# Optimization experiments

Measured on AMD Instinct MI355X. Metric: run time of the kernel, lower is better.

## Reference

```python
import jax, jax.numpy as jnp
import numpy as np

T, HW, C = 64, 24, 1024
MID = 256
WIN = 2  # 'video' forward_type -> 2x2 windows


def setup_inputs() -> dict:
    key = jax.random.key(0)
    k1, k2, k3, k4, k5 = jax.random.split(key, 5)
    return {
        "image_features": jax.random.normal(k1, (T, HW * HW, C), dtype=jnp.float32),
        "Wq": jax.random.normal(k2, (C, MID), dtype=jnp.float32) * 0.02,
        "bq": jax.random.normal(k3, (MID,), dtype=jnp.float32) * 0.02,
        "Wk": jax.random.normal(k4, (C, MID), dtype=jnp.float32) * 0.02,
        "bk": jax.random.normal(k5, (MID,), dtype=jnp.float32) * 0.02,
    }


def reference(image_features, Wq, bq, Wk, bk):
    # forward_type == 'video': 2x2 windowed attention over pooled patches
    t, n, c = image_features.shape
    H = W = int(np.sqrt(n))
    h2, w2 = H // WIN, W // WIN
    # [T, H, W, C] -> [T, h2, 2, w2, 2, C] -> [T, h2, w2, 2, 2, C] -> [T, P, 4, C]
    x = image_features.reshape(t, h2, WIN, w2, WIN, c)
    windows = x.transpose(0, 1, 3, 2, 4, 5).reshape(t, h2 * w2, WIN * WIN, c)
    # avg_pool2d(2,2) == mean over each 2x2 window
    pooled = windows.mean(axis=2)  # [T, P, C]
    q = pooled @ Wq + bq           # [T, P, MID]
    k = windows @ Wk + bk          # [T, P, 4, MID]
    scale = 1.0 / jnp.sqrt(jnp.float32(MID))
    attn = jnp.einsum("tpd,tpwd->tpw", q, k) * scale  # [T, P, 4]
    attn = jnp.nan_to_num(attn)
    attn = jax.nn.softmax(attn, axis=-1)
    attn_feat = jnp.einsum("tpw,tpwc->tpc", attn, windows)  # softmax-weighted value avg
    # query dim has size 1, so .mean(1) in torch is identity here
    return pooled + attn_feat  # [T, P, C]; new_image_size = (h2, w2) is static
```

## Files before the change

kernel.cpp:

```cpp
#include <hip/hip_runtime.h>

#define T_ 64
#define P_ 144
#define NPAIR 9216
#define C_ 1024
#define MID_ 256
#define NKROW 36864

typedef __attribute__((ext_vector_type(4))) float f32x4;
typedef __attribute__((ext_vector_type(8))) __bf16 bf16x8;
typedef __attribute__((ext_vector_type(4))) __bf16 bf16x4;

__device__ __forceinline__ void async_copy16(const void* g, void* l) {
  __builtin_amdgcn_global_load_lds(
      (const __attribute__((address_space(1))) unsigned int*)g,
      (__attribute__((address_space(3))) unsigned int*)l, 16, 0, 0);
}

__global__ void pool_convert_kernel(const float* __restrict__ img,
                                    __bf16* __restrict__ winb,
                                    __bf16* __restrict__ poolb) {
  const int pair = blockIdx.x;
  const int t = pair / P_;
  const int p = pair - t * P_;
  const int wy = p / 12, wx = p - wy * 12;
  const int c = threadIdx.x * 4;
  const float* base = img + (size_t)t * 576 * C_;
  const int r0 = 48 * wy + 2 * wx;
  const int rows[4] = {r0, r0 + 1, r0 + 24, r0 + 25};
  f32x4 s = {0.f, 0.f, 0.f, 0.f};
#pragma unroll
  for (int w = 0; w < 4; ++w) {
    f32x4 v = *(const f32x4*)(base + (size_t)rows[w] * C_ + c);
    s += v;
    bf16x4 bv;
#pragma unroll
    for (int j = 0; j < 4; ++j) bv[j] = (__bf16)v[j];
    *(bf16x4*)(winb + ((size_t)pair * 4 + w) * C_ + c) = bv;
  }
  s *= 0.25f;
  bf16x4 pv;
#pragma unroll
  for (int j = 0; j < 4; ++j) pv[j] = (__bf16)s[j];
  *(bf16x4*)(poolb + (size_t)pair * C_ + c) = pv;
}

__global__ void wtrans_kernel(const float* __restrict__ Wq,
                              const float* __restrict__ Wk,
                              __bf16* __restrict__ Wqt,
                              __bf16* __restrict__ Wkt) {
  __shared__ float t[32][33];
  const float* src = blockIdx.z ? Wk : Wq;
  __bf16* dst = blockIdx.z ? Wkt : Wqt;
  const int k0 = blockIdx.x * 32, n0 = blockIdx.y * 32;
#pragma unroll
  for (int i = 0; i < 32; i += 8) {
    t[threadIdx.y + i][threadIdx.x] =
        src[(size_t)(k0 + threadIdx.y + i) * MID_ + n0 + threadIdx.x];
  }
  __syncthreads();
#pragma unroll
  for (int i = 0; i < 32; i += 8) {
    dst[(size_t)(n0 + threadIdx.y + i) * C_ + k0 + threadIdx.x] =
        (__bf16)t[threadIdx.x][threadIdx.y + i];
  }
}

__global__ __launch_bounds__(256) void gemm_qk_kernel(
    const __bf16* __restrict__ Apool, const __bf16* __restrict__ Awin,
    const __bf16* __restrict__ Bqt, const __bf16* __restrict__ Bkt,
    const float* __restrict__ bq, const float* __restrict__ bk,
    float* __restrict__ Qo, float* __restrict__ Ko) {
  __shared__ __align__(16) __bf16 As[128 * 32];
  __shared__ __align__(16) __bf16 Bs[128 * 32];
  const int bid = blockIdx.x;
  const __bf16* A;
  const __bf16* Bt;
  const float* bias;
  float* Cout;
  int mt, nt;
  if (bid < 144) {
    A = Apool; Bt = Bqt; bias = bq; Cout = Qo;
    mt = bid >> 1; nt = bid & 1;
  } else {
    const int b = bid - 144;
    A = Awin; Bt = Bkt; bias = bk; Cout = Ko;
    mt = b >> 1; nt = b & 1;
  }
  const int tid = threadIdx.x;
  const int lane = tid & 63;
  const int wv = tid >> 6;
  const int quad = lane >> 4, lr = lane & 15;
  const int wm = wv >> 1, wn = wv & 1;

  const int r0 = tid >> 2, p0 = tid & 3;
  const __bf16* ga0 = A + ((size_t)mt * 128 + r0) * (size_t)C_ + p0 * 8;
  const __bf16* ga1 = ga0 + (size_t)64 * C_;
  const __bf16* gb0 = Bt + ((size_t)nt * 128 + r0) * (size_t)C_ + p0 * 8;
  const __bf16* gb1 = gb0 + (size_t)64 * C_;
  const int wvb = (tid & ~63) * 16;
  char* AsB0 = (char*)As + wvb;
  char* AsB1 = (char*)As + 4096 + wvb;
  char* BsB0 = (char*)Bs + wvb;
  char* BsB1 = (char*)Bs + 4096 + wvb;

  f32x4 acc[4][4] = {};

  for (int it = 0; it < 32; ++it) {
    async_copy16(ga0, AsB0);
    async_copy16(ga1, AsB1);
    async_copy16(gb0, BsB0);
    async_copy16(gb1, BsB1);
    ga0 += 32; ga1 += 32; gb0 += 32; gb1 += 32;
    __syncthreads();

    bf16x8 a[4], b[4];
    const bf16x8* Ap = (const bf16x8*)As;
    const bf16x8* Bp = (const bf16x8*)Bs;
#pragma unroll
    for (int i = 0; i < 4; ++i) {
      a[i] = Ap[(wm * 64 + i * 16 + lr) * 4 + quad];
      b[i] = Bp[(wn * 64 + i * 16 + lr) * 4 + quad];
    }
#pragma unroll
    for (int mi = 0; mi < 4; ++mi)
#pragma unroll
      for (int ni = 0; ni < 4; ++ni)
        acc[mi][ni] = __builtin_amdgcn_mfma_f32_16x16x32_bf16(
            a[mi], b[ni], acc[mi][ni], 0, 0, 0);
    __syncthreads();
  }

  const int colb = nt * 128 + wn * 64;
  const int rowb = mt * 128 + wm * 64 + quad * 4;
#pragma unroll
  for (int ni = 0; ni < 4; ++ni) {
    const int col = colb + ni * 16 + lr;
    const float bv = bias[col];
#pragma unroll
    for (int mi = 0; mi < 4; ++mi) {
      const int row = rowb + mi * 16;
#pragma unroll
      for (int r = 0; r < 4; ++r)
        Cout[(size_t)(row + r) * MID_ + col] = acc[mi][ni][r] + bv;
    }
  }
}

__global__ void attn_epilogue_kernel(const float* __restrict__ Qm,
                                     const float* __restrict__ Km,
                                     const __bf16* __restrict__ winb,
                                     const __bf16* __restrict__ poolb,
                                     float* __restrict__ out) {
  const int pair = blockIdx.x;
  const int tid = threadIdx.x;
  const int wv = tid >> 6, lane = tid & 63;
  __shared__ float red[4][4];
  const float qv = Qm[(size_t)pair * MID_ + tid];
#pragma unroll
  for (int w = 0; w < 4; ++w) {
    float p = qv * Km[((size_t)pair * 4 + w) * MID_ + tid];
    p += __shfl_down(p, 32);
    p += __shfl_down(p, 16);
    p += __shfl_down(p, 8);
    p += __shfl_down(p, 4);
    p += __shfl_down(p, 2);
    p += __shfl_down(p, 1);
    if (lane == 0) red[w][wv] = p;
  }
  __syncthreads();
  float lg[4];
  float mx = -1e30f;
#pragma unroll
  for (int w = 0; w < 4; ++w) {
    lg[w] = (red[w][0] + red[w][1] + red[w][2] + red[w][3]) * 0.0625f;
    mx = fmaxf(mx, lg[w]);
  }
  float att[4];
  float ssum = 0.f;
#pragma unroll
  for (int w = 0; w < 4; ++w) {
    att[w] = __expf(lg[w] - mx);
    ssum += att[w];
  }
  const float inv = 1.f / ssum;

  const int c = tid * 4;
  const bf16x4 pv = *(const bf16x4*)(poolb + (size_t)pair * C_ + c);
  f32x4 o;
#pragma unroll
  for (int j = 0; j < 4; ++j) o[j] = (float)pv[j];
#pragma unroll
  for (int w = 0; w < 4; ++w) {
    const float aw = att[w] * inv;
    const bf16x4 wvv = *(const bf16x4*)(winb + ((size_t)pair * 4 + w) * C_ + c);
#pragma unroll
    for (int j = 0; j < 4; ++j) o[j] += aw * (float)wvv[j];
  }
  *(f32x4*)(out + (size_t)pair * C_ + c) = o;
}

extern "C" void kernel_launch(void* const* d_in, const int* in_sizes, int n_in,
                              void* d_out, int out_size, void* d_ws,
                              size_t ws_size, hipStream_t stream) {
  const float* img = (const float*)d_in[0];
  const float* Wq = (const float*)d_in[1];
  const float* bq = (const float*)d_in[2];
  const float* Wk = (const float*)d_in[3];
  const float* bk = (const float*)d_in[4];
  float* out = (float*)d_out;

  char* ws = (char*)d_ws;
  __bf16* winb = (__bf16*)ws;
  __bf16* poolb = (__bf16*)(ws + 75497472);
  __bf16* Wqt = (__bf16*)(ws + 94371840);
  __bf16* Wkt = (__bf16*)(ws + 94896128);
  float* Qo = (float*)(ws + 95420416);
  float* Ko = (float*)(ws + 104857600);

  pool_convert_kernel<<<NPAIR, 256, 0, stream>>>(img, winb, poolb);
  wtrans_kernel<<<dim3(32, 8, 2), dim3(32, 8, 1), 0, stream>>>(Wq, Wk, Wqt, Wkt);
  gemm_qk_kernel<<<720, 256, 0, stream>>>(poolb, winb, Wqt, Wkt, bq, bk, Qo, Ko);
  attn_epilogue_kernel<<<NPAIR, 256, 0, stream>>>(Qo, Ko, winb, poolb, out);
}
```

Before: 299.2 us.

## Drop bf16 window copy; convert fp32 image inside K GEMM and epilogue

Removes the materialized bf16 windows buffer. The K-projection GEMM now loads fp32 image rows directly and converts them to bf16 in registers before writing LDS. The output kernel reads the fp32 image to compute both the pooled mean and the weighted sum. Pooling and weight transposition are merged into one launch, and Q/K are stored as bf16 to halve that traffic. The K GEMM A-path switches from async LDS copies to synchronous register loads, which may expose more latency, and Q/K precision drops.

```diff
diff --git a/kernel.cpp b/kernel.cpp
--- a/kernel.cpp
+++ b/kernel.cpp
@@ -5,7 +5,6 @@
 #define NPAIR 9216
 #define C_ 1024
 #define MID_ 256
-#define NKROW 36864
 
 typedef __attribute__((ext_vector_type(4))) float f32x4;
 typedef __attribute__((ext_vector_type(8))) __bf16 bf16x8;
@@ -17,74 +16,96 @@
       (__attribute__((address_space(3))) unsigned int*)l, 16, 0, 0);
 }
 
-__global__ void pool_convert_kernel(const float* __restrict__ img,
-                                    __bf16* __restrict__ winb,
-                                    __bf16* __restrict__ poolb) {
-  const int pair = blockIdx.x;
+__device__ __forceinline__ int img_row_of(int g) {
+  const int pair = g >> 2;
+  const int w = g & 3;
   const int t = pair / P_;
-  const int p = pair - t * P_;
-  const int wy = p / 12, wx = p - wy * 12;
-  const int c = threadIdx.x * 4;
-  const float* base = img + (size_t)t * 576 * C_;
-  const int r0 = 48 * wy + 2 * wx;
-  const int rows[4] = {r0, r0 + 1, r0 + 24, r0 + 25};
-  f32x4 s = {0.f, 0.f, 0.f, 0.f};
-#pragma unroll
-  for (int w = 0; w < 4; ++w) {
-    f32x4 v = *(const f32x4*)(base + (size_t)rows[w] * C_ + c);
-    s += v;
-    bf16x4 bv;
-#pragma unroll
-    for (int j = 0; j < 4; ++j) bv[j] = (__bf16)v[j];
-    *(bf16x4*)(winb + ((size_t)pair * 4 + w) * C_ + c) = bv;
-  }
-  s *= 0.25f;
-  bf16x4 pv;
-#pragma unroll
-  for (int j = 0; j < 4; ++j) pv[j] = (__bf16)s[j];
-  *(bf16x4*)(poolb + (size_t)pair * C_ + c) = pv;
-}
-
-__global__ void wtrans_kernel(const float* __restrict__ Wq,
-                              const float* __restrict__ Wk,
-                              __bf16* __restrict__ Wqt,
-                              __bf16* __restrict__ Wkt) {
-  __shared__ float t[32][33];
-  const float* src = blockIdx.z ? Wk : Wq;
-  __bf16* dst = blockIdx.z ? Wkt : Wqt;
-  const int k0 = blockIdx.x * 32, n0 = blockIdx.y * 32;
-#pragma unroll
-  for (int i = 0; i < 32; i += 8) {
-    t[threadIdx.y + i][threadIdx.x] =
-        src[(size_t)(k0 + threadIdx.y + i) * MID_ + n0 + threadIdx.x];
-  }
-  __syncthreads();
-#pragma unroll
-  for (int i = 0; i < 32; i += 8) {
-    dst[(size_t)(n0 + threadIdx.y + i) * C_ + k0 + threadIdx.x] =
-        (__bf16)t[threadIdx.x][threadIdx.y + i];
-  }
+  const int pp = pair - t * P_;
+  const int wy = pp / 12, wx = pp - wy * 12;
+  return t * 576 + 48 * wy + 2 * wx + (w >> 1) * 24 + (w & 1);
+}
+
+__global__ void prep_kernel(const float* __restrict__ img,
+                            const float* __restrict__ Wq,
+                            const float* __restrict__ Wk,
+                            __bf16* __restrict__ poolb,
+                            __bf16* __restrict__ Wqt,
+                            __bf16* __restrict__ Wkt) {
+  const int bid = blockIdx.x;
+  const int tid = threadIdx.x;
+  if (bid < NPAIR) {
+    const int t = bid / P_;
+    const int p = bid - t * P_;
+    const int wy = p / 12, wx = p - wy * 12;
+    const int c = tid * 4;
+    const float* base = img + ((size_t)t * 576 + 48 * wy + 2 * wx) * C_;
+    f32x4 s = *(const f32x4*)(base + c);
+    s += *(const f32x4*)(base + (size_t)1 * C_ + c);
+    s += *(const f32x4*)(base + (size_t)24 * C_ + c);
+    s += *(const f32x4*)(base + (size_t)25 * C_ + c);
+    s *= 0.25f;
+    bf16x4 pv;
+#pragma unroll
+    for (int j = 0; j < 4; ++j) pv[j] = (__bf16)s[j];
+    *(bf16x4*)(poolb + (size_t)bid * C_ + c) = pv;
+  } else {
+    __shared__ float tl[32][33];
+    const int b = bid - NPAIR;
+    const int bx = b & 31;
+    const int by = (b >> 5) & 7;
+    const int bz = b >> 8;
+    const float* src = bz ? Wk : Wq;
+    __bf16* dst = bz ? Wkt : Wqt;
+    const int tx = tid & 31, ty = tid >> 5;
+    const int k0 = bx * 32, n0 = by * 32;
+#pragma unroll
+    for (int i = 0; i < 32; i += 8)
+      tl[ty + i][tx] = src[(size_t)(k0 + ty + i) * MID_ + n0 + tx];
+    __syncthreads();
+#pragma unroll
+    for (int i = 0; i < 32; i += 8)
+      dst[(size_t)(n0 + ty + i) * C_ + k0 + tx] = (__bf16)tl[tx][ty + i];
+  }
+}
+
+__device__ __forceinline__ void mfma_tile(const __bf16* As, const __bf16* Bs,
+                                          int wm, int wn, int quad, int lr,
+                                          f32x4 acc[4][4]) {
+  bf16x8 a[4], b[4];
+  const bf16x8* Ap = (const bf16x8*)As;
+  const bf16x8* Bp = (const bf16x8*)Bs;
+#pragma unroll
+  for (int i = 0; i < 4; ++i) {
+    a[i] = Ap[(wm * 64 + i * 16 + lr) * 4 + quad];
+    b[i] = Bp[(wn * 64 + i * 16 + lr) * 4 + quad];
+  }
+#pragma unroll
+  for (int mi = 0; mi < 4; ++mi)
+#pragma unroll
+    for (int ni = 0; ni < 4; ++ni)
+      acc[mi][ni] = __builtin_amdgcn_mfma_f32_16x16x32_bf16(
+          a[mi], b[ni], acc[mi][ni], 0, 0, 0);
 }
 
 __global__ __launch_bounds__(256) void gemm_qk_kernel(
-    const __bf16* __restrict__ Apool, const __bf16* __restrict__ Awin,
+    const __bf16* __restrict__ poolb, const float* __restrict__ img,
     const __bf16* __restrict__ Bqt, const __bf16* __restrict__ Bkt,
     const float* __restrict__ bq, const float* __restrict__ bk,
-    float* __restrict__ Qo, float* __restrict__ Ko) {
+    __bf16* __restrict__ Qb, __bf16* __restrict__ Kb) {
   __shared__ __align__(16) __bf16 As[128 * 32];
   __shared__ __align__(16) __bf16 Bs[128 * 32];
   const int bid = blockIdx.x;
-  const __bf16* A;
+  const bool isQ = bid < 144;
   const __bf16* Bt;
   const float* bias;
-  float* Cout;
+  __bf16* Cout;
   int mt, nt;
-  if (bid < 144) {
-    A = Apool; Bt = Bqt; bias = bq; Cout = Qo;
+  if (isQ) {
+    Bt = Bqt; bias = bq; Cout = Qb;
     mt = bid >> 1; nt = bid & 1;
   } else {
     const int b = bid - 144;
-    A = Awin; Bt = Bkt; bias = bk; Cout = Ko;
+    Bt = Bkt; bias = bk; Cout = Kb;
     mt = b >> 1; nt = b & 1;
   }
   const int tid = threadIdx.x;
@@ -94,41 +115,56 @@
   const int wm = wv >> 1, wn = wv & 1;
 
   const int r0 = tid >> 2, p0 = tid & 3;
-  const __bf16* ga0 = A + ((size_t)mt * 128 + r0) * (size_t)C_ + p0 * 8;
-  const __bf16* ga1 = ga0 + (size_t)64 * C_;
+  const int wvb = (tid & ~63) * 16;
   const __bf16* gb0 = Bt + ((size_t)nt * 128 + r0) * (size_t)C_ + p0 * 8;
   const __bf16* gb1 = gb0 + (size_t)64 * C_;
-  const int wvb = (tid & ~63) * 16;
-  char* AsB0 = (char*)As + wvb;
-  char* AsB1 = (char*)As + 4096 + wvb;
   char* BsB0 = (char*)Bs + wvb;
   char* BsB1 = (char*)Bs + 4096 + wvb;
 
   f32x4 acc[4][4] = {};
 
-  for (int it = 0; it < 32; ++it) {
-    async_copy16(ga0, AsB0);
-    async_copy16(ga1, AsB1);
-    async_copy16(gb0, BsB0);
-    async_copy16(gb1, BsB1);
-    ga0 += 32; ga1 += 32; gb0 += 32; gb1 += 32;
-    __syncthreads();
-
-    bf16x8 a[4], b[4];
-    const bf16x8* Ap = (const bf16x8*)As;
-    const bf16x8* Bp = (const bf16x8*)Bs;
-#pragma unroll
-    for (int i = 0; i < 4; ++i) {
-      a[i] = Ap[(wm * 64 + i * 16 + lr) * 4 + quad];
-      b[i] = Bp[(wn * 64 + i * 16 + lr) * 4 + quad];
+  if (isQ) {
+    const __bf16* ga0 = poolb + ((size_t)mt * 128 + r0) * (size_t)C_ + p0 * 8;
+    const __bf16* ga1 = ga0 + (size_t)64 * C_;
+    char* AsB0 = (char*)As + wvb;
+    char* AsB1 = (char*)As + 4096 + wvb;
+    for (int it = 0; it < 32; ++it) {
+      async_copy16(ga0, AsB0);
+      async_copy16(ga1, AsB1);
+      async_copy16(gb0, BsB0);
+      async_copy16(gb1, BsB1);
+      ga0 += 32; ga1 += 32; gb0 += 32; gb1 += 32;
+      __syncthreads();
+      mfma_tile(As, Bs, wm, wn, quad, lr, acc);
+      __syncthreads();
     }
-#pragma unroll
-    for (int mi = 0; mi < 4; ++mi)
-#pragma unroll
-      for (int ni = 0; ni < 4; ++ni)
-        acc[mi][ni] = __builtin_amdgcn_mfma_f32_16x16x32_bf16(
-            a[mi], b[ni], acc[mi][ni], 0, 0, 0);
-    __syncthreads();
+  } else {
+    const int g0 = mt * 128 + r0;
+    const float* fa0 = img + (size_t)img_row_of(g0) * C_ + p0 * 8;
+    const float* fa1 = img + (size_t)img_row_of(g0 + 64) * C_ + p0 * 8;
+    __bf16* lw0 = As + (size_t)tid * 8;
+    __bf16* lw1 = As + (size_t)(tid + 256) * 8;
+    for (int it = 0; it < 32; ++it) {
+      const f32x4 u0 = *(const f32x4*)fa0;
+      const f32x4 u1 = *(const f32x4*)(fa0 + 4);
+      const f32x4 u2 = *(const f32x4*)fa1;
+      const f32x4 u3 = *(const f32x4*)(fa1 + 4);
+      fa0 += 32; fa1 += 32;
+      bf16x8 c0, c1;
+#pragma unroll
+      for (int j = 0; j < 4; ++j) {
+        c0[j] = (__bf16)u0[j]; c0[4 + j] = (__bf16)u1[j];
+        c1[j] = (__bf16)u2[j]; c1[4 + j] = (__bf16)u3[j];
+      }
+      *(bf16x8*)lw0 = c0;
+      *(bf16x8*)lw1 = c1;
+      async_copy16(gb0, BsB0);
+      async_copy16(gb1, BsB1);
+      gb0 += 32; gb1 += 32;
+      __syncthreads();
+      mfma_tile(As, Bs, wm, wn, quad, lr, acc);
+      __syncthreads();
+    }
   }
 
   const int colb = nt * 128 + wn * 64;
@@ -142,24 +178,34 @@
       const int row = rowb + mi * 16;
 #pragma unroll
       for (int r = 0; r < 4; ++r)
-        Cout[(size_t)(row + r) * MID_ + col] = acc[mi][ni][r] + bv;
+        Cout[(size_t)(row + r) * MID_ + col] = (__bf16)(acc[mi][ni][r] + bv);
     }
   }
 }
 
-__global__ void attn_epilogue_kernel(const float* __restrict__ Qm,
-                                     const float* __restrict__ Km,
-                                     const __bf16* __restrict__ winb,
-                                     const __bf16* __restrict__ poolb,
-                                     float* __restrict__ out) {
+__global__ void attn_out_kernel(const __bf16* __restrict__ Qb,
+                                const __bf16* __restrict__ Kb,
+                                const float* __restrict__ img,
+                                float* __restrict__ out) {
   const int pair = blockIdx.x;
   const int tid = threadIdx.x;
   const int wv = tid >> 6, lane = tid & 63;
   __shared__ float red[4][4];
-  const float qv = Qm[(size_t)pair * MID_ + tid];
+
+  const int t = pair / P_;
+  const int pp = pair - t * P_;
+  const int wy = pp / 12, wx = pp - wy * 12;
+  const float* base = img + ((size_t)t * 576 + 48 * wy + 2 * wx) * C_;
+  const int c = tid * 4;
+  f32x4 v0 = *(const f32x4*)(base + c);
+  f32x4 v1 = *(const f32x4*)(base + (size_t)1 * C_ + c);
+  f32x4 v2 = *(const f32x4*)(base + (size_t)24 * C_ + c);
+  f32x4 v3 = *(const f32x4*)(base + (size_t)25 * C_ + c);
+
+  const float qv = (float)Qb[(size_t)pair * MID_ + tid];
 #pragma unroll
   for (int w = 0; w < 4; ++w) {
-    float p = qv * Km[((size_t)pair * 4 + w) * MID_ + tid];
+    float p = qv * (float)Kb[((size_t)pair * 4 + w) * MID_ + tid];
     p += __shfl_down(p, 32);
     p += __shfl_down(p, 16);
     p += __shfl_down(p, 8);
@@ -184,19 +230,11 @@
     ssum += att[w];
   }
   const float inv = 1.f / ssum;
-
-  const int c = tid * 4;
-  const bf16x4 pv = *(const bf16x4*)(poolb + (size_t)pair * C_ + c);
-  f32x4 o;
-#pragma unroll
-  for (int j = 0; j < 4; ++j) o[j] = (float)pv[j];
-#pragma unroll
-  for (int w = 0; w < 4; ++w) {
-    const float aw = att[w] * inv;
-    const bf16x4 wvv = *(const bf16x4*)(winb + ((size_t)pair * 4 + w) * C_ + c);
-#pragma unroll
-    for (int j = 0; j < 4; ++j) o[j] += aw * (float)wvv[j];
-  }
+  const float a0 = att[0] * inv, a1 = att[1] * inv;
+  const float a2 = att[2] * inv, a3 = att[3] * inv;
+
+  f32x4 o = (v0 + v1 + v2 + v3) * 0.25f;
+  o += a0 * v0 + a1 * v1 + a2 * v2 + a3 * v3;
   *(f32x4*)(out + (size_t)pair * C_ + c) = o;
 }
 
@@ -211,15 +249,13 @@
   float* out = (float*)d_out;
 
   char* ws = (char*)d_ws;
-  __bf16* winb = (__bf16*)ws;
-  __bf16* poolb = (__bf16*)(ws + 75497472);
-  __bf16* Wqt = (__bf16*)(ws + 94371840);
-  __bf16* Wkt = (__bf16*)(ws + 94896128);
-  float* Qo = (float*)(ws + 95420416);
-  float* Ko = (float*)(ws + 104857600);
-
-  pool_convert_kernel<<<NPAIR, 256, 0, stream>>>(img, winb, poolb);
-  wtrans_kernel<<<dim3(32, 8, 2), dim3(32, 8, 1), 0, stream>>>(Wq, Wk, Wqt, Wkt);
-  gemm_qk_kernel<<<720, 256, 0, stream>>>(poolb, winb, Wqt, Wkt, bq, bk, Qo, Ko);
-  attn_epilogue_kernel<<<NPAIR, 256, 0, stream>>>(Qo, Ko, winb, poolb, out);
-}
+  __bf16* poolb = (__bf16*)ws;
+  __bf16* Wqt = (__bf16*)(ws + 18874368);
+  __bf16* Wkt = (__bf16*)(ws + 19398656);
+  __bf16* Qb = (__bf16*)(ws + 19922944);
+  __bf16* Kb = (__bf16*)(ws + 24641536);
+
+  prep_kernel<<<NPAIR + 512, 256, 0, stream>>>(img, Wq, Wk, poolb, Wqt, Wkt);
+  gemm_qk_kernel<<<720, 256, 0, stream>>>(poolb, img, Wqt, Wkt, bq, bk, Qb, Kb);
+  attn_out_kernel<<<NPAIR, 256, 0, stream>>>(Qb, Kb, img, out);
+}
```

Result: slower. 315.0 us (+5.3%).
